# Kernel tuning notes

Hardware: AMD Instinct MI355X
Metric: run time of the kernel (lower is better)

Reference implementation:

```python
import jax, jax.numpy as jnp
import numpy as np

NUM_HEADS = 4
HEAD_DIM = 64  # out_dim // num_heads = 256 // 4
NEG_SLOPE = 0.2


def setup_inputs() -> dict:
    key = jax.random.key(0)
    k1, k2 = jax.random.split(key)
    h = jax.random.normal(k1, (8, 2048, 256), dtype=jnp.float32)
    # Linear(in_dim, head_dim*num_heads, bias=False): store as [in_dim, out_dim]
    W = jax.random.normal(k2, (256, 256), dtype=jnp.float32) * (1.0 / np.sqrt(256.0))
    return {"h": h, "W": W}


def reference(h, W):
    B, T, _ = h.shape
    # Wh: (B, H, T, D)
    Wh = (h @ W).reshape(B, T, NUM_HEADS, HEAD_DIM).transpose(0, 2, 1, 3)
    scale = 1.0 / (HEAD_DIM ** 0.5)
    # full T x T scores per head, LeakyReLU then softmax over keys
    scores = jnp.einsum('bhtd,bhsd->bhts', Wh, Wh) * scale
    attention = jax.nn.softmax(jax.nn.leaky_relu(scores, negative_slope=NEG_SLOPE), axis=-1)
    h_prime = jnp.einsum('bhts,bhsd->bhtd', attention, Wh)
    # concat=True: (B, T, H*D)
    return h_prime.transpose(0, 2, 1, 3).reshape(B, T, NUM_HEADS * HEAD_DIM)
```

## Files before the change

kernel.cpp:

```cpp
#include <hip/hip_runtime.h>

#define T_SEQ 2048
#define NH 4
#define DH 64

typedef __bf16 bf16x8 __attribute__((ext_vector_type(8)));
typedef float f32x4 __attribute__((ext_vector_type(4)));
typedef unsigned short u16x8 __attribute__((ext_vector_type(8)));

__device__ __forceinline__ unsigned short f2bf_rne(float x) {
  unsigned int u = __builtin_bit_cast(unsigned int, x);
  u += 0x7fffu + ((u >> 16) & 1u);
  return (unsigned short)(u >> 16);
}

__device__ __forceinline__ void async_cp16(const unsigned short* g, unsigned short* l) {
  __builtin_amdgcn_global_load_lds(
      (const __attribute__((address_space(1))) unsigned int*)g,
      (__attribute__((address_space(3))) unsigned int*)l, 16, 0, 0);
}

__global__ __launch_bounds__(256) void wprep(const float* __restrict__ W,
                                             unsigned short* __restrict__ Wt) {
  int tid = blockIdx.x * 256 + threadIdx.x;
  int k = tid >> 8, n = tid & 255;
  float w = W[tid];
  unsigned int u = __builtin_bit_cast(unsigned int, w);
  Wt[n * 256 + k] = (unsigned short)(u >> 16);
  float lo = w - __builtin_bit_cast(float, u & 0xffff0000u);
  Wt[65536 + n * 256 + k] =
      (unsigned short)(__builtin_bit_cast(unsigned int, lo) >> 16);
}

__global__ __launch_bounds__(256, 2) void wh_gemm(
    const float* __restrict__ h, const unsigned short* __restrict__ Wt,
    unsigned short* __restrict__ Kb, unsigned short* __restrict__ Vt) {
  __shared__ __align__(16) unsigned short Ahi[32 * 256];
  __shared__ __align__(16) unsigned short Alo[32 * 256];
  const int tid = threadIdx.x;
  const int wave = tid >> 6;
  const int lane = tid & 63;
  const int l15 = lane & 15;
  const int quad = lane >> 4;
  const int mbase = blockIdx.x * 32;
  const int col0 = wave * 64;

  {
    const int r = tid >> 3;
    const int cbase = (tid & 7) * 4;
    const float4* hp = (const float4*)(h + ((size_t)(mbase + r) << 8) + cbase * 8);
#pragma unroll
    for (int j = 0; j < 4; j++) {
      float4 f0 = hp[2 * j];
      float4 f1 = hp[2 * j + 1];
      u16x8 hi, lo;
#define SPLIT1(v, idx)                                                    \
  {                                                                       \
    unsigned int u_ = __builtin_bit_cast(unsigned int, (v));              \
    hi[idx] = (unsigned short)(u_ >> 16);                                 \
    float r_ = (v) - __builtin_bit_cast(float, u_ & 0xffff0000u);         \
    lo[idx] = (unsigned short)(__builtin_bit_cast(unsigned int, r_) >> 16); \
  }
      SPLIT1(f0.x, 0) SPLIT1(f0.y, 1) SPLIT1(f0.z, 2) SPLIT1(f0.w, 3)
      SPLIT1(f1.x, 4) SPLIT1(f1.y, 5) SPLIT1(f1.z, 6) SPLIT1(f1.w, 7)
#undef SPLIT1
      const int chunk = (cbase + j) ^ (r & 7);
      *(u16x8*)&Ahi[r * 256 + chunk * 8] = hi;
      *(u16x8*)&Alo[r * 256 + chunk * 8] = lo;
    }
  }
  __syncthreads();

  f32x4 acc[2][4];
#pragma unroll
  for (int mt = 0; mt < 2; mt++)
#pragma unroll
    for (int nt = 0; nt < 4; nt++) acc[mt][nt] = (f32x4){0.f, 0.f, 0.f, 0.f};

#pragma unroll 2
  for (int ks = 0; ks < 8; ks++) {
    const int k0 = ks * 32 + quad * 8;
    bf16x8 ahi[2], alo[2];
#pragma unroll
    for (int mt = 0; mt < 2; mt++) {
      const int row = mt * 16 + l15;
      const int ch = (ks * 4 + quad) ^ (row & 7);
      ahi[mt] = *(const bf16x8*)&Ahi[row * 256 + ch * 8];
      alo[mt] = *(const bf16x8*)&Alo[row * 256 + ch * 8];
    }
#pragma unroll
    for (int nt = 0; nt < 4; nt++) {
      const unsigned short* wp = Wt + ((size_t)(col0 + nt * 16 + l15) << 8) + k0;
      bf16x8 bhi = *(const bf16x8*)wp;
      bf16x8 blo = *(const bf16x8*)(wp + 65536);
#pragma unroll
      for (int mt = 0; mt < 2; mt++) {
        acc[mt][nt] = __builtin_amdgcn_mfma_f32_16x16x32_bf16(ahi[mt], bhi, acc[mt][nt], 0, 0, 0);
        acc[mt][nt] = __builtin_amdgcn_mfma_f32_16x16x32_bf16(alo[mt], bhi, acc[mt][nt], 0, 0, 0);
        acc[mt][nt] = __builtin_amdgcn_mfma_f32_16x16x32_bf16(ahi[mt], blo, acc[mt][nt], 0, 0, 0);
      }
    }
  }

  const float s1 = 0.424664717f;
#pragma unroll
  for (int mt = 0; mt < 2; mt++) {
    int row = mbase + mt * 16 + quad * 4;
    int b = row >> 11;
    int tb = row & 2047;
    size_t bh = (size_t)(b * NH + wave);
#pragma unroll
    for (int nt = 0; nt < 4; nt++) {
      int d = nt * 16 + l15;
      Kb[(bh * T_SEQ + tb + 0) * DH + d] = f2bf_rne(acc[mt][nt][0] * s1);
      Kb[(bh * T_SEQ + tb + 1) * DH + d] = f2bf_rne(acc[mt][nt][1] * s1);
      Kb[(bh * T_SEQ + tb + 2) * DH + d] = f2bf_rne(acc[mt][nt][2] * s1);
      Kb[(bh * T_SEQ + tb + 3) * DH + d] = f2bf_rne(acc[mt][nt][3] * s1);
      ushort4 vp;
      vp.x = f2bf_rne(acc[mt][nt][0]);
      vp.y = f2bf_rne(acc[mt][nt][1]);
      vp.z = f2bf_rne(acc[mt][nt][2]);
      vp.w = f2bf_rne(acc[mt][nt][3]);
      *(ushort4*)&Vt[(bh * DH + d) * T_SEQ + tb] = vp;
    }
  }
}

__global__ __launch_bounds__(256, 4) void attn(
    const unsigned short* __restrict__ Kb, const unsigned short* __restrict__ Vt,
    float* __restrict__ out, int gbase) {
  __shared__ __align__(16) unsigned short ldsK[2][64 * 64];
  __shared__ __align__(16) unsigned short ldsV[2][64 * 64];
  __shared__ __align__(16) unsigned short ldsP[4][16 * 64];
  const int tid = threadIdx.x;
  const int wave = tid >> 6;
  const int lane = tid & 63;
  const int l15 = lane & 15;
  const int quad = lane >> 4;
  const int g = gbase + blockIdx.x;
  const int lbid = (g & 7) * 128 + (g >> 3);
  const int bh = lbid >> 5;
  const int qtile = lbid & 31;
  const unsigned short* Kbh = Kb + (size_t)bh * T_SEQ * DH;
  const unsigned short* Vbh = Vt + (size_t)bh * DH * T_SEQ;

  const int qrow = qtile * 64 + wave * 16 + l15;
  bf16x8 aq0 = *(const bf16x8*)&Kbh[qrow * DH + quad * 8];
  bf16x8 aq1 = *(const bf16x8*)&Kbh[qrow * DH + 32 + quad * 8];

  f32x4 o[4];
  float lsum[4];
#pragma unroll
  for (int i = 0; i < 4; i++) {
    o[i] = (f32x4){0.f, 0.f, 0.f, 0.f};
    lsum[i] = 0.f;
  }
  unsigned short* Pw = ldsP[wave];

  auto stage = [&](int t, int buf) {
#pragma unroll
    for (int i = 0; i < 2; i++) {
      int slot = i * 256 + tid;
      int r = slot >> 3;
      int c = (slot & 7) ^ (r & 7);
      async_cp16(&Kbh[(t * 64 + r) * DH + c * 8],
                 &ldsK[buf][(i * 256 + wave * 64) * 8]);
      async_cp16(&Vbh[(size_t)r * T_SEQ + t * 64 + c * 8],
                 &ldsV[buf][(i * 256 + wave * 64) * 8]);
    }
  };

  stage(0, 0);

  for (int kt = 0; kt < 32; kt++) {
    const int cur = kt & 1;
    if (kt < 31) {
      stage(kt + 1, cur ^ 1);
      asm volatile("s_waitcnt vmcnt(4)" ::: "memory");
    } else {
      asm volatile("s_waitcnt vmcnt(0)" ::: "memory");
    }
    __builtin_amdgcn_s_barrier();
    __builtin_amdgcn_sched_barrier(0);

    const unsigned short* Kl = ldsK[cur];
    const unsigned short* Vl = ldsV[cur];

    f32x4 sfr[4];
    __builtin_amdgcn_s_setprio(1);
#pragma unroll
    for (int nt = 0; nt < 4; nt++) {
      int key = nt * 16 + l15;
      bf16x8 kf0 = *(const bf16x8*)&Kl[key * 64 + ((quad ^ (key & 7)) << 3)];
      bf16x8 kf1 = *(const bf16x8*)&Kl[key * 64 + (((4 + quad) ^ (key & 7)) << 3)];
      f32x4 s = {0.f, 0.f, 0.f, 0.f};
      s = __builtin_amdgcn_mfma_f32_16x16x32_bf16(aq0, kf0, s, 0, 0, 0);
      s = __builtin_amdgcn_mfma_f32_16x16x32_bf16(aq1, kf1, s, 0, 0, 0);
      sfr[nt] = s;
    }
    __builtin_amdgcn_s_setprio(0);

#pragma unroll
    for (int nt = 0; nt < 4; nt++) {
      int col = nt * 16 + l15;
#pragma unroll
      for (int reg = 0; reg < 4; reg++) {
        float v = sfr[nt][reg];
        float e = __builtin_amdgcn_exp2f(fmaxf(v, 0.2f * v));
        lsum[reg] += e;
        int row = quad * 4 + reg;
        Pw[(row << 6) + (((((col >> 3) ^ (row & 7))) << 3) | (col & 7))] =
            (unsigned short)(__builtin_bit_cast(unsigned int, e) >> 16);
      }
    }
    __builtin_amdgcn_s_waitcnt(0xC07F);

    __builtin_amdgcn_s_setprio(1);
#pragma unroll
    for (int kc = 0; kc < 2; kc++) {
      bf16x8 ap = *(const bf16x8*)&Pw[(l15 << 6) + ((((kc << 2) + quad) ^ (l15 & 7)) << 3)];
#pragma unroll
      for (int nt = 0; nt < 4; nt++) {
        int d = nt * 16 + l15;
        bf16x8 vf = *(const bf16x8*)&Vl[(d << 6) + ((((kc << 2) + quad) ^ (d & 7)) << 3)];
        o[nt] = __builtin_amdgcn_mfma_f32_16x16x32_bf16(ap, vf, o[nt], 0, 0, 0);
      }
    }
    __builtin_amdgcn_s_setprio(0);
    __builtin_amdgcn_sched_barrier(0);
    __builtin_amdgcn_s_barrier();
  }

  float inv[4];
#pragma unroll
  for (int reg = 0; reg < 4; reg++) {
    float l = lsum[reg];
    l += __shfl_xor(l, 1, 64);
    l += __shfl_xor(l, 2, 64);
    l += __shfl_xor(l, 4, 64);
    l += __shfl_xor(l, 8, 64);
    inv[reg] = 1.0f / l;
  }
  const int b = bh >> 2, head = bh & 3;
#pragma unroll
  for (int nt = 0; nt < 4; nt++) {
    int d = nt * 16 + l15;
#pragma unroll
    for (int reg = 0; reg < 4; reg++) {
      int trow = qtile * 64 + wave * 16 + quad * 4 + reg;
      out[((size_t)b * T_SEQ + trow) * 256 + head * 64 + d] = o[nt][reg] * inv[reg];
    }
  }
}

extern "C" void kernel_launch(void* const* d_in, const int* in_sizes, int n_in,
                              void* d_out, int out_size, void* d_ws, size_t ws_size,
                              hipStream_t stream) {
  const float* h = (const float*)d_in[0];
  const float* W = (const float*)d_in[1];
  float* out = (float*)d_out;
  unsigned short* Kb = (unsigned short*)d_ws;
  unsigned short* Vt = Kb + (size_t)32 * T_SEQ * DH;
  unsigned short* Wt = Vt + (size_t)32 * T_SEQ * DH;
  wprep<<<256, 256, 0, stream>>>(W, Wt);
  wh_gemm<<<512, 256, 0, stream>>>(h, Wt, Kb, Vt);
  attn<<<512, 256, 0, stream>>>(Kb, Vt, out, 0);
  attn<<<512, 256, 0, stream>>>(Kb, Vt, out, 512);
}
```

Before: 165.1 us.

## Process two 16-row query tiles per wave to reuse K/V tiles

Each wave now handles 32 query rows (two MFMA M-tiles) instead of 16, so every block covers 128 queries and each K/V LDS tile is reused twice as much. The grid drops from two 512-block launches to a single 512-block launch, which halves global-to-LDS staging traffic and removes one launch. The P scratch buffer doubles and register use rises (launch bounds lowered from 4 to 3 blocks per CU), which may cut occupancy and latency hiding.

Result: faster. 149.3 us (-9.5%).

```diff
diff --git a/kernel.cpp b/kernel.cpp
--- a/kernel.cpp
+++ b/kernel.cpp
@@ -126,35 +126,41 @@
   }
 }
 
-__global__ __launch_bounds__(256, 4) void attn(
+__global__ __launch_bounds__(256, 3) void attn(
     const unsigned short* __restrict__ Kb, const unsigned short* __restrict__ Vt,
-    float* __restrict__ out, int gbase) {
+    float* __restrict__ out) {
   __shared__ __align__(16) unsigned short ldsK[2][64 * 64];
   __shared__ __align__(16) unsigned short ldsV[2][64 * 64];
-  __shared__ __align__(16) unsigned short ldsP[4][16 * 64];
+  __shared__ __align__(16) unsigned short ldsP[4][32 * 64];
   const int tid = threadIdx.x;
   const int wave = tid >> 6;
   const int lane = tid & 63;
   const int l15 = lane & 15;
   const int quad = lane >> 4;
-  const int g = gbase + blockIdx.x;
-  const int lbid = (g & 7) * 128 + (g >> 3);
-  const int bh = lbid >> 5;
-  const int qtile = lbid & 31;
+  const int lbid = (blockIdx.x & 7) * 64 + (blockIdx.x >> 3);
+  const int bh = lbid >> 4;
+  const int qtile = lbid & 15;
   const unsigned short* Kbh = Kb + (size_t)bh * T_SEQ * DH;
   const unsigned short* Vbh = Vt + (size_t)bh * DH * T_SEQ;
 
-  const int qrow = qtile * 64 + wave * 16 + l15;
-  bf16x8 aq0 = *(const bf16x8*)&Kbh[qrow * DH + quad * 8];
-  bf16x8 aq1 = *(const bf16x8*)&Kbh[qrow * DH + 32 + quad * 8];
-
-  f32x4 o[4];
-  float lsum[4];
-#pragma unroll
-  for (int i = 0; i < 4; i++) {
-    o[i] = (f32x4){0.f, 0.f, 0.f, 0.f};
-    lsum[i] = 0.f;
-  }
+  const int qbase = qtile * 128 + wave * 32;
+  bf16x8 aq[2][2];
+#pragma unroll
+  for (int mt = 0; mt < 2; mt++) {
+    const unsigned short* qp = &Kbh[(qbase + mt * 16 + l15) * DH + quad * 8];
+    aq[mt][0] = *(const bf16x8*)qp;
+    aq[mt][1] = *(const bf16x8*)(qp + 32);
+  }
+
+  f32x4 o[2][4];
+  float lsum[2][4];
+#pragma unroll
+  for (int mt = 0; mt < 2; mt++)
+#pragma unroll
+    for (int i = 0; i < 4; i++) {
+      o[mt][i] = (f32x4){0.f, 0.f, 0.f, 0.f};
+      lsum[mt][i] = 0.f;
+    }
   unsigned short* Pw = ldsP[wave];
 
   auto stage = [&](int t, int buf) {
@@ -186,44 +192,52 @@
     const unsigned short* Kl = ldsK[cur];
     const unsigned short* Vl = ldsV[cur];
 
-    f32x4 sfr[4];
+    f32x4 sfr[2][4];
     __builtin_amdgcn_s_setprio(1);
 #pragma unroll
     for (int nt = 0; nt < 4; nt++) {
       int key = nt * 16 + l15;
       bf16x8 kf0 = *(const bf16x8*)&Kl[key * 64 + ((quad ^ (key & 7)) << 3)];
       bf16x8 kf1 = *(const bf16x8*)&Kl[key * 64 + (((4 + quad) ^ (key & 7)) << 3)];
-      f32x4 s = {0.f, 0.f, 0.f, 0.f};
-      s = __builtin_amdgcn_mfma_f32_16x16x32_bf16(aq0, kf0, s, 0, 0, 0);
-      s = __builtin_amdgcn_mfma_f32_16x16x32_bf16(aq1, kf1, s, 0, 0, 0);
-      sfr[nt] = s;
+#pragma unroll
+      for (int mt = 0; mt < 2; mt++) {
+        f32x4 s = {0.f, 0.f, 0.f, 0.f};
+        s = __builtin_amdgcn_mfma_f32_16x16x32_bf16(aq[mt][0], kf0, s, 0, 0, 0);
+        s = __builtin_amdgcn_mfma_f32_16x16x32_bf16(aq[mt][1], kf1, s, 0, 0, 0);
+        sfr[mt][nt] = s;
+      }
     }
     __builtin_amdgcn_s_setprio(0);
 
 #pragma unroll
-    for (int nt = 0; nt < 4; nt++) {
-      int col = nt * 16 + l15;
-#pragma unroll
-      for (int reg = 0; reg < 4; reg++) {
-        float v = sfr[nt][reg];
-        float e = __builtin_amdgcn_exp2f(fmaxf(v, 0.2f * v));
-        lsum[reg] += e;
-        int row = quad * 4 + reg;
-        Pw[(row << 6) + (((((col >> 3) ^ (row & 7))) << 3) | (col & 7))] =
-            (unsigned short)(__builtin_bit_cast(unsigned int, e) >> 16);
-      }
-    }
+    for (int mt = 0; mt < 2; mt++)
+#pragma unroll
+      for (int nt = 0; nt < 4; nt++) {
+        int col = nt * 16 + l15;
+#pragma unroll
+        for (int reg = 0; reg < 4; reg++) {
+          float v = sfr[mt][nt][reg];
+          float e = __builtin_amdgcn_exp2f(fmaxf(v, 0.2f * v));
+          lsum[mt][reg] += e;
+          int row = mt * 16 + quad * 4 + reg;
+          Pw[(row << 6) + (((((col >> 3) ^ (row & 7))) << 3) | (col & 7))] =
+              (unsigned short)(__builtin_bit_cast(unsigned int, e) >> 16);
+        }
+      }
     __builtin_amdgcn_s_waitcnt(0xC07F);
 
     __builtin_amdgcn_s_setprio(1);
 #pragma unroll
     for (int kc = 0; kc < 2; kc++) {
-      bf16x8 ap = *(const bf16x8*)&Pw[(l15 << 6) + ((((kc << 2) + quad) ^ (l15 & 7)) << 3)];
+      const int pch = (((kc << 2) + quad) ^ (l15 & 7)) << 3;
+      bf16x8 ap0 = *(const bf16x8*)&Pw[(l15 << 6) + pch];
+      bf16x8 ap1 = *(const bf16x8*)&Pw[((16 + l15) << 6) + pch];
 #pragma unroll
       for (int nt = 0; nt < 4; nt++) {
         int d = nt * 16 + l15;
         bf16x8 vf = *(const bf16x8*)&Vl[(d << 6) + ((((kc << 2) + quad) ^ (d & 7)) << 3)];
-        o[nt] = __builtin_amdgcn_mfma_f32_16x16x32_bf16(ap, vf, o[nt], 0, 0, 0);
+        o[0][nt] = __builtin_amdgcn_mfma_f32_16x16x32_bf16(ap0, vf, o[0][nt], 0, 0, 0);
+        o[1][nt] = __builtin_amdgcn_mfma_f32_16x16x32_bf16(ap1, vf, o[1][nt], 0, 0, 0);
       }
     }
     __builtin_amdgcn_s_setprio(0);
@@ -231,24 +245,27 @@
     __builtin_amdgcn_s_barrier();
   }
 
-  float inv[4];
-#pragma unroll
-  for (int reg = 0; reg < 4; reg++) {
-    float l = lsum[reg];
-    l += __shfl_xor(l, 1, 64);
-    l += __shfl_xor(l, 2, 64);
-    l += __shfl_xor(l, 4, 64);
-    l += __shfl_xor(l, 8, 64);
-    inv[reg] = 1.0f / l;
-  }
   const int b = bh >> 2, head = bh & 3;
 #pragma unroll
-  for (int nt = 0; nt < 4; nt++) {
-    int d = nt * 16 + l15;
+  for (int mt = 0; mt < 2; mt++) {
+    float inv[4];
 #pragma unroll
     for (int reg = 0; reg < 4; reg++) {
-      int trow = qtile * 64 + wave * 16 + quad * 4 + reg;
-      out[((size_t)b * T_SEQ + trow) * 256 + head * 64 + d] = o[nt][reg] * inv[reg];
+      float l = lsum[mt][reg];
+      l += __shfl_xor(l, 1, 64);
+      l += __shfl_xor(l, 2, 64);
+      l += __shfl_xor(l, 4, 64);
+      l += __shfl_xor(l, 8, 64);
+      inv[reg] = 1.0f / l;
+    }
+#pragma unroll
+    for (int nt = 0; nt < 4; nt++) {
+      int d = nt * 16 + l15;
+#pragma unroll
+      for (int reg = 0; reg < 4; reg++) {
+        int trow = qbase + mt * 16 + quad * 4 + reg;
+        out[((size_t)b * T_SEQ + trow) * 256 + head * 64 + d] = o[mt][nt][reg] * inv[reg];
+      }
     }
   }
 }
@@ -264,6 +281,5 @@
   unsigned short* Wt = Vt + (size_t)32 * T_SEQ * DH;
   wprep<<<256, 256, 0, stream>>>(W, Wt);
   wh_gemm<<<512, 256, 0, stream>>>(h, Wt, Kb, Vt);
-  attn<<<512, 256, 0, stream>>>(Kb, Vt, out, 0);
-  attn<<<512, 256, 0, stream>>>(Kb, Vt, out, 512);
-}
+  attn<<<512, 256, 0, stream>>>(Kb, Vt, out);
+}
```
